# Performance work log

Hardware: AMD Instinct MI355X
Metric: run time of the kernel (lower is better)

## Reference

```python
import jax, jax.numpy as jnp
import numpy as np

B, T, DIM = 4, 1024, 2048
H, KVH = 16, 4
HD = DIM // H          # 128
G = H // KVH           # GQA group size = 4


def setup_inputs() -> dict:
    key = jax.random.key(0)
    ks = jax.random.split(key, 4)
    s = 1.0 / np.sqrt(DIM)
    x = jax.random.normal(ks[0], (B, T, DIM), jnp.float32)
    Wq = jax.random.normal(ks[1], (DIM, DIM), jnp.float32) * s
    Wkv = jax.random.normal(ks[2], (DIM, 2 * KVH * HD), jnp.float32) * s
    Wo = jax.random.normal(ks[3], (DIM, DIM), jnp.float32) * s
    # RoPE tables (theta=10000, half-split / rotate-half convention)
    inv_freq = 1.0 / (10000.0 ** (np.arange(0, HD, 2, dtype=np.float64) / HD))
    freqs = np.outer(np.arange(T, dtype=np.float64), inv_freq)  # [T, HD/2]
    cos = jnp.asarray(np.cos(freqs), jnp.float32)
    sin = jnp.asarray(np.sin(freqs), jnp.float32)
    return {"x": x, "Wq": Wq, "Wkv": Wkv, "Wo": Wo, "cos": cos, "sin": sin}


def _rope(u, cos, sin):
    # u: [B,T,heads,HD]; cos/sin: [T, HD/2]
    u1, u2 = jnp.split(u, 2, axis=-1)
    c = cos[None, :, None, :]
    s = sin[None, :, None, :]
    return jnp.concatenate([u1 * c - u2 * s, u1 * s + u2 * c], axis=-1)


def reference(x, Wq, Wkv, Wo, cos, sin):
    Bs, Ts, C = x.shape
    q = (x @ Wq).reshape(Bs, Ts, H, HD)
    kv = (x @ Wkv).reshape(Bs, Ts, 2, KVH, HD)
    k, v = kv[:, :, 0], kv[:, :, 1]
    q = _rope(q, cos, sin)
    k = _rope(k, cos, sin)
    # GQA without materializing repeated K/V: fold group dim into q
    qg = q.reshape(Bs, Ts, KVH, G, HD)
    scores = jnp.einsum('bqhgd,bkhd->bhgqk', qg, k) / np.float32(np.sqrt(HD))
    causal = jnp.tril(jnp.ones((Ts, Ts), bool))
    neg = jnp.finfo(scores.dtype).min
    scores = jnp.where(causal, scores, neg)
    att = jax.nn.softmax(scores, axis=-1)
    out = jnp.einsum('bhgqk,bkhd->bqhgd', att, v).reshape(Bs, Ts, C)
    return out @ Wo
```

## Files before the change

### kernel.cpp

```cpp
#include <hip/hip_runtime.h>

typedef unsigned short u16;
typedef unsigned int u32;
typedef __bf16 bf16x8 __attribute__((ext_vector_type(8)));
typedef float f32x4 __attribute__((ext_vector_type(4)));

#define BB   4
#define TT   1024
#define CDIM 2048
#define NH   16
#define NKV  4
#define HDIM 128

__device__ __forceinline__ float b2f(u16 u) {
    union { u32 i; float f; } x; x.i = ((u32)u) << 16; return x.f;
}
__device__ __forceinline__ u16 f2b(float f) {
    union { float f; u32 i; } x; x.f = f;
    u32 r = (x.i + 0x7fffu + ((x.i >> 16) & 1u)) >> 16;
    return (u16)r;
}
__device__ __forceinline__ void async16(const void* g, void* l) {
    __builtin_amdgcn_global_load_lds((const __attribute__((address_space(1))) void*)g,
                                     (__attribute__((address_space(3))) void*)l, 16, 0, 0);
}

__device__ __forceinline__ bool wave_is_f32(const u16* xp) {
    u16 v = xp[(threadIdx.x & 63) * 2];
    int e = (v >> 7) & 0xFF;
    bool bad = (v != 0) && (e < 90 || e > 160);
    return __popcll(__ballot(bad)) > 16;
}

__global__ __launch_bounds__(256) void pre_k(const void* __restrict__ x,
                                             const void* __restrict__ Wq,
                                             const void* __restrict__ Wkv,
                                             const void* __restrict__ Wo,
                                             u16* __restrict__ xb,
                                             u16* __restrict__ csb,
                                             u16* __restrict__ snb,
                                             u16* __restrict__ WqkvT,
                                             u16* __restrict__ WoT,
                                             const void* __restrict__ cs,
                                             const void* __restrict__ sn) {
    const bool f32m = wave_is_f32((const u16*)x);
    int bid = blockIdx.x;
    if (bid < 8320) {
        const void* src; u16* dst; int i;
        if (bid < 8192)      { src = x;  dst = xb;  i = bid * 256 + threadIdx.x; }
        else if (bid < 8256) { src = cs; dst = csb; i = (bid - 8192) * 256 + threadIdx.x; }
        else                 { src = sn; dst = snb; i = (bid - 8256) * 256 + threadIdx.x; }
        union { u16 u[4]; ushort4 v; } o;
        if (f32m) {
            float4 f = ((const float4*)src)[i];
            o.u[0] = f2b(f.x); o.u[1] = f2b(f.y); o.u[2] = f2b(f.z); o.u[3] = f2b(f.w);
        } else {
            o.v = ((const ushort4*)src)[i];
        }
        ((ushort4*)dst)[i] = o.v;
        return;
    }
    __shared__ alignas(16) u16 tile[64 * 65];
    int t = bid - 8320;
    const void* W; u16* WT; int rows, cols, bx, by;
    if (t < 1024)      { W = Wq;  WT = WqkvT;                    rows = 2048; cols = 2048; bx = t & 31;  by = t >> 5; }
    else if (t < 1536) { int l = t - 1024; W = Wkv; WT = WqkvT + (long)2048 * 2048; rows = 2048; cols = 1024; bx = l & 15; by = l >> 4; }
    else               { int l = t - 1536; W = Wo;  WT = WoT;  rows = 2048; cols = 2048; bx = l & 31;   by = l >> 5; }
    const int r0 = by * 64, c0 = bx * 64;
#pragma unroll
    for (int i = 0; i < 16; i++) {
        int c = threadIdx.x + i * 256;
        int rr = c >> 6, cc = c & 63;
        long idx = (long)(r0 + rr) * cols + c0 + cc;
        tile[rr * 65 + cc] = f32m ? f2b(((const float*)W)[idx]) : ((const u16*)W)[idx];
    }
    __syncthreads();
#pragma unroll
    for (int i = 0; i < 16; i++) {
        int c = threadIdx.x + i * 256;
        int rr = c >> 6, cc = c & 63;
        WT[(long)(c0 + rr) * rows + r0 + cc] = tile[cc * 65 + rr];
    }
}

__global__ __launch_bounds__(256) void gemm_bt(const u16* __restrict__ A,
                                               const u16* __restrict__ Bt,
                                               void* __restrict__ C,
                                               int M, int N, int Kd,
                                               const u16* __restrict__ xprobe) {
    __shared__ alignas(16) u16 As[128 * 32];
    __shared__ alignas(16) u16 Bs[128 * 32];
    const bool f32m = (xprobe != nullptr) && wave_is_f32(xprobe);
    const int tid = threadIdx.x;
    const int w = tid >> 6, lane = tid & 63;
    const int wm = w >> 1, wn = w & 1;
    const int l16 = lane & 15, quad = lane >> 4;
    const int bm = blockIdx.y, bn = blockIdx.x;
    const long arow0 = (long)bm * 128;
    const long brow0 = (long)bn * 128;
    const int srow = lane >> 2;
    const int schunk = lane & 3;

    f32x4 acc[4][4];
#pragma unroll
    for (int i = 0; i < 4; i++)
#pragma unroll
        for (int j = 0; j < 4; j++) acc[i][j] = {0.f, 0.f, 0.f, 0.f};

    for (int k0 = 0; k0 < Kd; k0 += 32) {
        __syncthreads();
#pragma unroll
        for (int j = 0; j < 2; j++) {
            int r0 = w * 32 + j * 16;
            const u16* gA = A + (arow0 + r0 + srow) * Kd + k0 + schunk * 8;
            async16(gA, &As[r0 * 32]);
            const u16* gB = Bt + (brow0 + r0 + srow) * Kd + k0 + schunk * 8;
            async16(gB, &Bs[r0 * 32]);
        }
        __syncthreads();
        bf16x8 af[4], bfr[4];
#pragma unroll
        for (int mt = 0; mt < 4; mt++)
            af[mt] = *(const bf16x8*)&As[(wm * 64 + mt * 16 + l16) * 32 + quad * 8];
#pragma unroll
        for (int nt = 0; nt < 4; nt++)
            bfr[nt] = *(const bf16x8*)&Bs[(wn * 64 + nt * 16 + l16) * 32 + quad * 8];
#pragma unroll
        for (int mt = 0; mt < 4; mt++)
#pragma unroll
            for (int nt = 0; nt < 4; nt++)
                acc[mt][nt] = __builtin_amdgcn_mfma_f32_16x16x32_bf16(
                    af[mt], bfr[nt], acc[mt][nt], 0, 0, 0);
    }
#pragma unroll
    for (int mt = 0; mt < 4; mt++) {
#pragma unroll
        for (int nt = 0; nt < 4; nt++) {
            int col = bn * 128 + wn * 64 + nt * 16 + l16;
#pragma unroll
            for (int r = 0; r < 4; r++) {
                long row = bm * 128 + wm * 64 + mt * 16 + quad * 4 + r;
                if (f32m) ((float*)C)[row * N + col] = acc[mt][nt][r];
                else      ((u16*)C)[row * N + col] = f2b(acc[mt][nt][r]);
            }
        }
    }
}

__global__ __launch_bounds__(256) void prep_k(const u16* __restrict__ QKVraw,
                                              const u16* __restrict__ cs,
                                              const u16* __restrict__ sn,
                                              u16* __restrict__ Qr,
                                              u16* __restrict__ Kr,
                                              u16* __restrict__ Vt) {
    int bid = blockIdx.x;
    if (bid < 16384) {
        int idx = bid * 256 + threadIdx.x;
        int d = idx & 63;
        int t = (idx >> 6) & (TT - 1);
        int bh = idx >> 16;
        long src = ((long)((bh >> 4) * TT + t)) * 3072 + (bh & 15) * HDIM;
        float u1 = b2f(QKVraw[src + d]), u2 = b2f(QKVraw[src + d + 64]);
        float c = b2f(cs[t * 64 + d]), s = b2f(sn[t * 64 + d]);
        long dst = ((long)bh * TT + t) * HDIM;
        Qr[dst + d] = f2b(u1 * c - u2 * s);
        Qr[dst + d + 64] = f2b(u1 * s + u2 * c);
    } else if (bid < 20480) {
        int idx = (bid - 16384) * 256 + threadIdx.x;
        int d = idx & 63;
        int t = (idx >> 6) & (TT - 1);
        int bk = idx >> 16;
        long src = ((long)((bk >> 2) * TT + t)) * 3072 + 2048 + (bk & 3) * HDIM;
        float u1 = b2f(QKVraw[src + d]), u2 = b2f(QKVraw[src + d + 64]);
        float c = b2f(cs[t * 64 + d]), s = b2f(sn[t * 64 + d]);
        long dst = ((long)bk * TT + t) * HDIM;
        Kr[dst + d] = f2b(u1 * c - u2 * s);
        Kr[dst + d + 64] = f2b(u1 * s + u2 * c);
    } else {
        int idx = (bid - 20480) * 256 + threadIdx.x;
        int t = idx & (TT - 1);
        int d = (idx >> 10) & (HDIM - 1);
        int bk = idx >> 17;
        Vt[idx] = QKVraw[((long)(bk >> 2) * TT + t) * 3072 + 2560 + (bk & 3) * HDIM + d];
    }
}

__global__ __launch_bounds__(256) void attn_kernel(const u16* __restrict__ Q,
                                                   const u16* __restrict__ Kr,
                                                   const u16* __restrict__ Vt,
                                                   u16* __restrict__ O) {
    __shared__ alignas(16) u16 Ks[2][64 * 128];
    __shared__ alignas(16) u16 Vts[2][128 * 64];
    __shared__ alignas(16) u16 Ps[64 * 88];

    const int tid = threadIdx.x, w = tid >> 6, lane = tid & 63;
    const int l16 = lane & 15, quad = lane >> 4;
    const float scale2 = 0.08838834764831845f * 1.4426950408889634f;

#pragma unroll 1
    for (int it = 0; it < 2; it++) {
        const int j = it ? (1023 - (int)blockIdx.x) : (int)blockIdx.x;
        const int qt = 15 - (j >> 6);
        const int bh = j & 63;
        const int b = bh >> 4, h = bh & 15;
        const int kvh = h >> 2;
        const long qrow0 = (long)bh * TT + qt * 64;
        const long krow0 = (long)(b * NKV + kvh) * TT;
        const long vbase = ((long)(b * NKV + kvh) * HDIM) * TT;

        __syncthreads();

#pragma unroll
        for (int i = 0; i < 4; i++) {
            int slot0 = (w * 4 + i) * 64;
            int slot = slot0 + lane;
            int row = slot >> 4, cp = slot & 15;
            int cg = (cp & 8) | ((cp ^ row) & 7);
            async16(Q + (qrow0 + row) * HDIM + cg * 8, &Ks[0][slot0 * 8]);
        }
        asm volatile("s_waitcnt vmcnt(0)" ::: "memory");
        bf16x8 qf[4];
        {
            const int Rq = w * 16 + l16;
#pragma unroll
            for (int ds = 0; ds < 4; ds++) {
                int c = ds * 4 + quad;
                qf[ds] = *(const bf16x8*)&Ks[0][Rq * 128 + ((c & 8) | ((c ^ Rq) & 7)) * 8];
            }
        }
        asm volatile("s_waitcnt lgkmcnt(0)" ::: "memory");

#pragma unroll
        for (int i = 0; i < 4; i++) {
            int slot0 = (w * 4 + i) * 64;
            int slot = slot0 + lane;
            int row = slot >> 4, cp = slot & 15;
            int cg = (cp & 8) | ((cp ^ row) & 7);
            async16(Kr + (krow0 + row) * HDIM + cg * 8, &Ks[0][slot0 * 8]);
        }
#pragma unroll
        for (int i = 0; i < 4; i++) {
            int slot0 = (w * 4 + i) * 64;
            int slot = slot0 + lane;
            int row = slot >> 3, cp = slot & 7;
            int cg = cp ^ (row & 7);
            async16(Vt + vbase + (long)row * TT + cg * 8, &Vts[0][slot0 * 8]);
        }
        if (qt >= 1) {
#pragma unroll
            for (int i = 0; i < 4; i++) {
                int slot0 = (w * 4 + i) * 64;
                int slot = slot0 + lane;
                int row = slot >> 4, cp = slot & 15;
                int cg = (cp & 8) | ((cp ^ row) & 7);
                async16(Kr + (krow0 + 64 + row) * HDIM + cg * 8, &Ks[1][slot0 * 8]);
            }
#pragma unroll
            for (int i = 0; i < 4; i++) {
                int slot0 = (w * 4 + i) * 64;
                int slot = slot0 + lane;
                int row = slot >> 3, cp = slot & 7;
                int cg = cp ^ (row & 7);
                async16(Vt + vbase + (long)row * TT + 64 + cg * 8, &Vts[1][slot0 * 8]);
            }
            asm volatile("s_waitcnt vmcnt(8)" ::: "memory");
        } else {
            asm volatile("s_waitcnt vmcnt(0)" ::: "memory");
        }
        asm volatile("s_barrier" ::: "memory");

        f32x4 o[8];
#pragma unroll
        for (int i = 0; i < 8; i++) o[i] = {0.f, 0.f, 0.f, 0.f};
        float m_i = -1.0e30f, l_i = 0.f;
        const int qg = qt * 64 + w * 16 + l16;

#pragma unroll 1
        for (int kt = 0; kt <= qt; kt++) {
            const int cur = kt & 1;
            const u16* ksb = Ks[cur];
            const u16* vsb = Vts[cur];

            f32x4 s[4];
#pragma unroll
            for (int nt = 0; nt < 4; nt++) s[nt] = {0.f, 0.f, 0.f, 0.f};
#pragma unroll
            for (int ds = 0; ds < 4; ds++) {
                int c = ds * 4 + quad;
#pragma unroll
                for (int nt = 0; nt < 4; nt++) {
                    int Rk = nt * 16 + l16;
                    bf16x8 ak = *(const bf16x8*)&ksb[Rk * 128 + ((c & 8) | ((c ^ Rk) & 7)) * 8];
                    s[nt] = __builtin_amdgcn_mfma_f32_16x16x32_bf16(ak, qf[ds], s[nt], 0, 0, 0);
                }
            }

            float p[4][4];
            float mx = -1.0e30f;
            if (kt == qt) {
#pragma unroll
                for (int nt = 0; nt < 4; nt++)
#pragma unroll
                    for (int r = 0; r < 4; r++) {
                        int kcol = kt * 64 + nt * 16 + quad * 4 + r;
                        float v = (kcol <= qg) ? (float)s[nt][r] * scale2 : -1.0e30f;
                        p[nt][r] = v;
                        mx = fmaxf(mx, v);
                    }
            } else {
#pragma unroll
                for (int nt = 0; nt < 4; nt++)
#pragma unroll
                    for (int r = 0; r < 4; r++) {
                        float v = (float)s[nt][r] * scale2;
                        p[nt][r] = v;
                        mx = fmaxf(mx, v);
                    }
            }
            mx = fmaxf(mx, __shfl_xor(mx, 16));
            mx = fmaxf(mx, __shfl_xor(mx, 32));
            float mnew = fmaxf(m_i, mx);
            float alpha = exp2f(m_i - mnew);
            float rs = 0.f;
#pragma unroll
            for (int nt = 0; nt < 4; nt++)
#pragma unroll
                for (int r = 0; r < 4; r++) {
                    float e = exp2f(p[nt][r] - mnew);
                    p[nt][r] = e;
                    rs += e;
                }
            rs += __shfl_xor(rs, 16);
            rs += __shfl_xor(rs, 32);
            l_i = l_i * alpha + rs;

            u32* Psw = (u32*)Ps;
            int pb = (w * 16 + l16) * 44 + quad * 2;
#pragma unroll
            for (int nt = 0; nt < 4; nt++) {
                u32 lo = (u32)f2b(p[nt][0]) | ((u32)f2b(p[nt][1]) << 16);
                u32 hi = (u32)f2b(p[nt][2]) | ((u32)f2b(p[nt][3]) << 16);
                Psw[pb + nt * 8]     = lo;
                Psw[pb + nt * 8 + 1] = hi;
            }
            if (__ballot(mnew != m_i) != 0ULL) {
#pragma unroll
                for (int n8 = 0; n8 < 8; n8++)
#pragma unroll
                    for (int r = 0; r < 4; r++) o[n8][r] *= alpha;
            }
            m_i = mnew;

            asm volatile("s_waitcnt lgkmcnt(0)" ::: "memory");

#pragma unroll
            for (int ks = 0; ks < 2; ks++) {
                bf16x8 bp = *(const bf16x8*)&Ps[(w * 16 + l16) * 88 + ks * 32 + quad * 8];
#pragma unroll
                for (int n8 = 0; n8 < 8; n8++) {
                    int Rv = n8 * 16 + l16;
                    int c = ks * 4 + quad;
                    bf16x8 av = *(const bf16x8*)&vsb[Rv * 64 + (c ^ (Rv & 7)) * 8];
                    o[n8] = __builtin_amdgcn_mfma_f32_16x16x32_bf16(av, bp, o[n8], 0, 0, 0);
                }
            }

            if (kt == qt) break;

            asm volatile("s_waitcnt lgkmcnt(0)" ::: "memory");
            asm volatile("s_barrier" ::: "memory");
            if (kt + 2 <= qt) {
                const int nk = kt + 2;
#pragma unroll
                for (int i = 0; i < 4; i++) {
                    int slot0 = (w * 4 + i) * 64;
                    int slot = slot0 + lane;
                    int row = slot >> 4, cp = slot & 15;
                    int cg = (cp & 8) | ((cp ^ row) & 7);
                    async16(Kr + (krow0 + nk * 64 + row) * HDIM + cg * 8, &Ks[cur][slot0 * 8]);
                }
#pragma unroll
                for (int i = 0; i < 4; i++) {
                    int slot0 = (w * 4 + i) * 64;
                    int slot = slot0 + lane;
                    int row = slot >> 3, cp = slot & 7;
                    int cg = cp ^ (row & 7);
                    async16(Vt + vbase + (long)row * TT + nk * 64 + cg * 8, &Vts[cur][slot0 * 8]);
                }
                asm volatile("s_waitcnt vmcnt(8)" ::: "memory");
            } else {
                asm volatile("s_waitcnt vmcnt(0)" ::: "memory");
            }
            asm volatile("s_barrier" ::: "memory");
        }

        float inv = 1.0f / l_i;
        long obase = ((long)(b * TT + qg)) * CDIM + h * HDIM;
#pragma unroll
        for (int n8 = 0; n8 < 8; n8++) {
            ushort4 st;
            st.x = f2b(o[n8][0] * inv);
            st.y = f2b(o[n8][1] * inv);
            st.z = f2b(o[n8][2] * inv);
            st.w = f2b(o[n8][3] * inv);
            *(ushort4*)&O[obase + n8 * 16 + quad * 4] = st;
        }
    }
}

extern "C" void kernel_launch(void* const* d_in, const int* in_sizes, int n_in,
                              void* d_out, int out_size, void* d_ws, size_t ws_size,
                              hipStream_t stream) {
    const void* x   = d_in[0];
    const void* Wq  = d_in[1];
    const void* Wkv = d_in[2];
    const void* Wo  = d_in[3];
    const void* cs  = d_in[4];
    const void* sn  = d_in[5];

    char* ws = (char*)d_ws;
    const size_t NEED = 105119748;
    if (ws_size < NEED) return;

    u16* WqkvT = (u16*)(ws + 0);
    u16* WoT   = (u16*)(ws + 12582912);
    u16* QKVraw= (u16*)(ws + 20971520);
    u16* Qr    = (u16*)(ws + 46137344);
    u16* Kr    = (u16*)(ws + 62914560);
    u16* Vt    = (u16*)(ws + 67108864);
    u16* ATT   = (u16*)(ws + 71303168);
    u16* xb    = (u16*)(ws + 88080384);
    u16* csb   = (u16*)(ws + 104857600);
    u16* snb   = (u16*)(ws + 104988672);

    pre_k<<<10880, 256, 0, stream>>>(x, Wq, Wkv, Wo, xb, csb, snb, WqkvT, WoT, cs, sn);

    gemm_bt<<<dim3(24, 32), 256, 0, stream>>>(xb, WqkvT, QKVraw, 4096, 3072, 2048, nullptr);

    prep_k<<<28672, 256, 0, stream>>>(QKVraw, csb, snb, Qr, Kr, Vt);

    attn_kernel<<<512, 256, 0, stream>>>(Qr, Kr, Vt, ATT);

    gemm_bt<<<dim3(16, 32), 256, 0, stream>>>(ATT, WoT, d_out, 4096, 2048, 2048, (const u16*)x);
}
```

Before: 330.1 us.

## Replace GEMM with 256x256 double-buffered swizzled MFMA kernel with phased prefetch

Swaps the 128x128, K=32 GEMM for a 512-thread kernel computing 256x256 tiles with K=64 steps. Loads are double-buffered through direct global-to-LDS copies with an XOR swizzle. Each K step is split into four MFMA phases that interleave LDS fragment reads with prefetch of the next A and B halves, using explicit waitcnt, barriers and priority hints. The aim is more reuse per loaded byte and overlapping memory traffic with matrix math. The trade-off is far fewer blocks than CUs for these shapes, and heavy LDS and register use.

```diff
diff --git a/kernel.cpp b/kernel.cpp
--- a/kernel.cpp
+++ b/kernel.cpp
@@ -83,63 +83,167 @@
     }
 }
 
-__global__ __launch_bounds__(256) void gemm_bt(const u16* __restrict__ A,
-                                               const u16* __restrict__ Bt,
-                                               void* __restrict__ C,
-                                               int M, int N, int Kd,
-                                               const u16* __restrict__ xprobe) {
-    __shared__ alignas(16) u16 As[128 * 32];
-    __shared__ alignas(16) u16 Bs[128 * 32];
+__global__ __launch_bounds__(512, 2) void gemm256(const u16* __restrict__ A,
+                                                  const u16* __restrict__ Bt,
+                                                  void* __restrict__ C,
+                                                  int M, int N, int Kd,
+                                                  const u16* __restrict__ xprobe) {
+    __shared__ alignas(16) u16 As[2][256 * 64];
+    __shared__ alignas(16) u16 Bs[2][256 * 64];
     const bool f32m = (xprobe != nullptr) && wave_is_f32(xprobe);
     const int tid = threadIdx.x;
     const int w = tid >> 6, lane = tid & 63;
-    const int wm = w >> 1, wn = w & 1;
+    const int wm = w >> 2, wn = w & 3;
     const int l16 = lane & 15, quad = lane >> 4;
-    const int bm = blockIdx.y, bn = blockIdx.x;
-    const long arow0 = (long)bm * 128;
-    const long brow0 = (long)bn * 128;
-    const int srow = lane >> 2;
-    const int schunk = lane & 3;
-
-    f32x4 acc[4][4];
-#pragma unroll
-    for (int i = 0; i < 4; i++)
+    const long arow0 = (long)blockIdx.y * 256;
+    const long brow0 = (long)blockIdx.x * 256;
+    const int NT = Kd >> 6;
+
+    long g0, g1;
+    int c0, c1;
+    {
+        int ch = w * 64 + lane;
+        int r = ch >> 3, cp = ch & 7;
+        g0 = (long)r * Kd + ((cp ^ (r & 7)) << 3);
+        c0 = (w * 64) << 3;
+        ch += 512;
+        r = ch >> 3; cp = ch & 7;
+        g1 = (long)r * Kd + ((cp ^ (r & 7)) << 3);
+        c1 = (512 + w * 64) << 3;
+    }
+    const u16* Ab = A + arow0 * Kd;
+    const u16* Bb = Bt + brow0 * Kd;
+    const long halfK = 128L * Kd;
+
+#define STAGE(ldsbase, gbase) do {      \
+        const u16* _g = (gbase);        \
+        u16* _l = (ldsbase);            \
+        async16(_g + g0, _l + c0);      \
+        async16(_g + g1, _l + c1); } while (0)
+
+    const int R0a = wm * 128 + l16, sA = R0a & 7;
+    const int R0b = wn * 64 + l16, sB = R0b & 7;
+    const int aoff[2] = { R0a * 64 + ((quad ^ sA) << 3), R0a * 64 + (((4 + quad) ^ sA) << 3) };
+    const int boff[2] = { R0b * 64 + ((quad ^ sB) << 3), R0b * 64 + (((4 + quad) ^ sB) << 3) };
+
+    f32x4 acc[8][4];
+#pragma unroll
+    for (int i = 0; i < 8; i++)
 #pragma unroll
         for (int j = 0; j < 4; j++) acc[i][j] = {0.f, 0.f, 0.f, 0.f};
 
-    for (int k0 = 0; k0 < Kd; k0 += 32) {
-        __syncthreads();
-#pragma unroll
-        for (int j = 0; j < 2; j++) {
-            int r0 = w * 32 + j * 16;
-            const u16* gA = A + (arow0 + r0 + srow) * Kd + k0 + schunk * 8;
-            async16(gA, &As[r0 * 32]);
-            const u16* gB = Bt + (brow0 + r0 + srow) * Kd + k0 + schunk * 8;
-            async16(gB, &Bs[r0 * 32]);
-        }
-        __syncthreads();
-        bf16x8 af[4], bfr[4];
-#pragma unroll
-        for (int mt = 0; mt < 4; mt++)
-            af[mt] = *(const bf16x8*)&As[(wm * 64 + mt * 16 + l16) * 32 + quad * 8];
-#pragma unroll
-        for (int nt = 0; nt < 4; nt++)
-            bfr[nt] = *(const bf16x8*)&Bs[(wn * 64 + nt * 16 + l16) * 32 + quad * 8];
-#pragma unroll
-        for (int mt = 0; mt < 4; mt++)
-#pragma unroll
-            for (int nt = 0; nt < 4; nt++)
-                acc[mt][nt] = __builtin_amdgcn_mfma_f32_16x16x32_bf16(
-                    af[mt], bfr[nt], acc[mt][nt], 0, 0, 0);
-    }
-#pragma unroll
-    for (int mt = 0; mt < 4; mt++) {
+    STAGE(&Bs[0][0], Bb);
+    STAGE(&Bs[0][128 * 64], Bb + halfK);
+    STAGE(&As[0][0], Ab);
+    STAGE(&As[0][128 * 64], Ab + halfK);
+    STAGE(&Bs[1][0], Bb + 64);
+    STAGE(&Bs[1][128 * 64], Bb + halfK + 64);
+    asm volatile("s_waitcnt vmcnt(4)" ::: "memory");
+    __builtin_amdgcn_s_barrier();
+
+#pragma unroll 1
+    for (int t = 0; t < NT; ++t) {
+        const int cur = t & 1, nxt = cur ^ 1;
+        const u16* pA = &As[cur][0];
+        const u16* pB = &Bs[cur][0];
+        bf16x8 afLo[4][2], afHi[4][2], bfA[2][2], bfB[2][2];
+
+#pragma unroll
+        for (int ks = 0; ks < 2; ks++) {
+#pragma unroll
+            for (int mt = 0; mt < 4; mt++)
+                afLo[mt][ks] = *(const bf16x8*)&pA[aoff[ks] + mt * 1024];
+#pragma unroll
+            for (int nt = 0; nt < 2; nt++)
+                bfA[nt][ks] = *(const bf16x8*)&pB[boff[ks] + nt * 1024];
+        }
+        if (t + 1 < NT) STAGE(&As[nxt][0], Ab + (t + 1) * 64);
+        __builtin_amdgcn_s_barrier();
+        asm volatile("s_waitcnt lgkmcnt(0)" ::: "memory");
+        __builtin_amdgcn_sched_barrier(0);
+        __builtin_amdgcn_s_setprio(1);
+#pragma unroll
+        for (int ks = 0; ks < 2; ks++)
+#pragma unroll
+            for (int mt = 0; mt < 4; mt++)
+#pragma unroll
+                for (int nt = 0; nt < 2; nt++)
+                    acc[mt][nt] = __builtin_amdgcn_mfma_f32_16x16x32_bf16(
+                        afLo[mt][ks], bfA[nt][ks], acc[mt][nt], 0, 0, 0);
+        __builtin_amdgcn_s_setprio(0);
+        __builtin_amdgcn_s_barrier();
+
+#pragma unroll
+        for (int ks = 0; ks < 2; ks++)
+#pragma unroll
+            for (int nt = 0; nt < 2; nt++)
+                bfB[nt][ks] = *(const bf16x8*)&pB[boff[ks] + (nt + 2) * 1024];
+        if (t + 1 < NT) STAGE(&As[nxt][128 * 64], Ab + halfK + (t + 1) * 64);
+        __builtin_amdgcn_s_barrier();
+        asm volatile("s_waitcnt lgkmcnt(0)" ::: "memory");
+        __builtin_amdgcn_sched_barrier(0);
+        __builtin_amdgcn_s_setprio(1);
+#pragma unroll
+        for (int ks = 0; ks < 2; ks++)
+#pragma unroll
+            for (int mt = 0; mt < 4; mt++)
+#pragma unroll
+                for (int nt = 0; nt < 2; nt++)
+                    acc[mt][nt + 2] = __builtin_amdgcn_mfma_f32_16x16x32_bf16(
+                        afLo[mt][ks], bfB[nt][ks], acc[mt][nt + 2], 0, 0, 0);
+        __builtin_amdgcn_s_setprio(0);
+        __builtin_amdgcn_s_barrier();
+
+#pragma unroll
+        for (int ks = 0; ks < 2; ks++)
+#pragma unroll
+            for (int mt = 0; mt < 4; mt++)
+                afHi[mt][ks] = *(const bf16x8*)&pA[aoff[ks] + (mt + 4) * 1024];
+        if (t + 2 < NT) STAGE(&Bs[cur][0], Bb + (t + 2) * 64);
+        __builtin_amdgcn_s_barrier();
+        asm volatile("s_waitcnt lgkmcnt(0)" ::: "memory");
+        __builtin_amdgcn_sched_barrier(0);
+        __builtin_amdgcn_s_setprio(1);
+#pragma unroll
+        for (int ks = 0; ks < 2; ks++)
+#pragma unroll
+            for (int mt = 0; mt < 4; mt++)
+#pragma unroll
+                for (int nt = 0; nt < 2; nt++)
+                    acc[mt + 4][nt + 2] = __builtin_amdgcn_mfma_f32_16x16x32_bf16(
+                        afHi[mt][ks], bfB[nt][ks], acc[mt + 4][nt + 2], 0, 0, 0);
+        __builtin_amdgcn_s_setprio(0);
+        __builtin_amdgcn_s_barrier();
+
+        if (t + 2 < NT) STAGE(&Bs[cur][128 * 64], Bb + halfK + (t + 2) * 64);
+        __builtin_amdgcn_s_barrier();
+        __builtin_amdgcn_sched_barrier(0);
+        __builtin_amdgcn_s_setprio(1);
+#pragma unroll
+        for (int ks = 0; ks < 2; ks++)
+#pragma unroll
+            for (int mt = 0; mt < 4; mt++)
+#pragma unroll
+                for (int nt = 0; nt < 2; nt++)
+                    acc[mt + 4][nt] = __builtin_amdgcn_mfma_f32_16x16x32_bf16(
+                        afHi[mt][ks], bfA[nt][ks], acc[mt + 4][nt], 0, 0, 0);
+        __builtin_amdgcn_s_setprio(0);
+        if (t + 1 < NT) {
+            if (t + 2 < NT) asm volatile("s_waitcnt vmcnt(4)" ::: "memory");
+            else            asm volatile("s_waitcnt vmcnt(0)" ::: "memory");
+            __builtin_amdgcn_s_barrier();
+        }
+    }
+#undef STAGE
+
+#pragma unroll
+    for (int mt = 0; mt < 8; mt++) {
 #pragma unroll
         for (int nt = 0; nt < 4; nt++) {
-            int col = bn * 128 + wn * 64 + nt * 16 + l16;
+            long col = brow0 + wn * 64 + nt * 16 + l16;
 #pragma unroll
             for (int r = 0; r < 4; r++) {
-                long row = bm * 128 + wm * 64 + mt * 16 + quad * 4 + r;
+                long row = arow0 + wm * 128 + mt * 16 + quad * 4 + r;
                 if (f32m) ((float*)C)[row * N + col] = acc[mt][nt][r];
                 else      ((u16*)C)[row * N + col] = f2b(acc[mt][nt][r]);
             }
@@ -435,11 +539,11 @@
 
     pre_k<<<10880, 256, 0, stream>>>(x, Wq, Wkv, Wo, xb, csb, snb, WqkvT, WoT, cs, sn);
 
-    gemm_bt<<<dim3(24, 32), 256, 0, stream>>>(xb, WqkvT, QKVraw, 4096, 3072, 2048, nullptr);
+    gemm256<<<dim3(12, 16), 512, 0, stream>>>(xb, WqkvT, QKVraw, 4096, 3072, 2048, nullptr);
 
     prep_k<<<28672, 256, 0, stream>>>(QKVraw, csb, snb, Qr, Kr, Vt);
 
     attn_kernel<<<512, 256, 0, stream>>>(Qr, Kr, Vt, ATT);
 
-    gemm_bt<<<dim3(16, 32), 256, 0, stream>>>(ATT, WoT, d_out, 4096, 2048, 2048, (const u16*)x);
-}
+    gemm256<<<dim3(8, 16), 512, 0, stream>>>(ATT, WoT, d_out, 4096, 2048, 2048, (const u16*)x);
+}
```

Measured after the change: 323.9 us. About the same (-1.9%).

## Rewrite GEMMs with double-buffered swizzled LDS, larger tiles and split MFMA phases

Applied to the files above, without the earlier changes.

Replaces the single-buffered 128x128, K=32 GEMM with a templated 512-thread kernel that uses K=64 tiles, double-buffered LDS with XOR swizzle, and manual vmcnt/barrier control. Global loads for the next-but-one tile are issued while MFMAs run in two halves, with s_setprio used to favour the math waves. The QKV projection uses 256x192 tiles and the output projection 128x256 tiles. This targets the GEMM loop's load latency and LDS bank conflicts, at the cost of more registers and LDS and fewer blocks (256 per GEMM), which may underfill the CUs.

```diff
diff --git a/kernel.cpp b/kernel.cpp
--- a/kernel.cpp
+++ b/kernel.cpp
@@ -23,6 +23,14 @@
 __device__ __forceinline__ void async16(const void* g, void* l) {
     __builtin_amdgcn_global_load_lds((const __attribute__((address_space(1))) void*)g,
                                      (__attribute__((address_space(3))) void*)l, 16, 0, 0);
+}
+template<int N> __device__ __forceinline__ void waitvm() {
+    static_assert(N == 0 || N == 3 || N == 4 || N == 6 || N == 7, "unsupported vmcnt");
+    if constexpr (N == 0)      asm volatile("s_waitcnt vmcnt(0)" ::: "memory");
+    else if constexpr (N == 3) asm volatile("s_waitcnt vmcnt(3)" ::: "memory");
+    else if constexpr (N == 4) asm volatile("s_waitcnt vmcnt(4)" ::: "memory");
+    else if constexpr (N == 6) asm volatile("s_waitcnt vmcnt(6)" ::: "memory");
+    else                       asm volatile("s_waitcnt vmcnt(7)" ::: "memory");
 }
 
 __device__ __forceinline__ bool wave_is_f32(const u16* xp) {
@@ -83,63 +91,145 @@
     }
 }
 
-__global__ __launch_bounds__(256) void gemm_bt(const u16* __restrict__ A,
-                                               const u16* __restrict__ Bt,
-                                               void* __restrict__ C,
-                                               int M, int N, int Kd,
-                                               const u16* __restrict__ xprobe) {
-    __shared__ alignas(16) u16 As[128 * 32];
-    __shared__ alignas(16) u16 Bs[128 * 32];
+template<int BM, int BN>
+__global__ __launch_bounds__(512, 2) void gemm_t(const u16* __restrict__ A,
+                                                 const u16* __restrict__ Bt,
+                                                 void* __restrict__ C,
+                                                 int N, int Kd,
+                                                 const u16* __restrict__ xprobe) {
+    constexpr int MF  = BM / 32;
+    constexpr int NF  = BN / 64;
+    constexpr int MF0 = MF / 2, MF1 = MF - MF0;
+    constexpr int NF0 = (NF + 1) / 2, NF1 = NF - NF0;
+    constexpr int NAU = BM / 64;
+    constexpr int NBU = BN / 64;
+
+    __shared__ alignas(16) u16 As[2][BM * 64];
+    __shared__ alignas(16) u16 Bs[2][BN * 64];
+
     const bool f32m = (xprobe != nullptr) && wave_is_f32(xprobe);
     const int tid = threadIdx.x;
     const int w = tid >> 6, lane = tid & 63;
-    const int wm = w >> 1, wn = w & 1;
+    const int wm = w >> 2, wn = w & 3;
     const int l16 = lane & 15, quad = lane >> 4;
-    const int bm = blockIdx.y, bn = blockIdx.x;
-    const long arow0 = (long)bm * 128;
-    const long brow0 = (long)bn * 128;
-    const int srow = lane >> 2;
-    const int schunk = lane & 3;
-
-    f32x4 acc[4][4];
-#pragma unroll
-    for (int i = 0; i < 4; i++)
-#pragma unroll
-        for (int j = 0; j < 4; j++) acc[i][j] = {0.f, 0.f, 0.f, 0.f};
-
-    for (int k0 = 0; k0 < Kd; k0 += 32) {
-        __syncthreads();
-#pragma unroll
-        for (int j = 0; j < 2; j++) {
-            int r0 = w * 32 + j * 16;
-            const u16* gA = A + (arow0 + r0 + srow) * Kd + k0 + schunk * 8;
-            async16(gA, &As[r0 * 32]);
-            const u16* gB = Bt + (brow0 + r0 + srow) * Kd + k0 + schunk * 8;
-            async16(gB, &Bs[r0 * 32]);
-        }
-        __syncthreads();
-        bf16x8 af[4], bfr[4];
-#pragma unroll
-        for (int mt = 0; mt < 4; mt++)
-            af[mt] = *(const bf16x8*)&As[(wm * 64 + mt * 16 + l16) * 32 + quad * 8];
-#pragma unroll
-        for (int nt = 0; nt < 4; nt++)
-            bfr[nt] = *(const bf16x8*)&Bs[(wn * 64 + nt * 16 + l16) * 32 + quad * 8];
-#pragma unroll
-        for (int mt = 0; mt < 4; mt++)
-#pragma unroll
-            for (int nt = 0; nt < 4; nt++)
-                acc[mt][nt] = __builtin_amdgcn_mfma_f32_16x16x32_bf16(
-                    af[mt], bfr[nt], acc[mt][nt], 0, 0, 0);
-    }
-#pragma unroll
-    for (int mt = 0; mt < 4; mt++) {
-#pragma unroll
-        for (int nt = 0; nt < 4; nt++) {
-            int col = bn * 128 + wn * 64 + nt * 16 + l16;
+    const long arow0 = (long)blockIdx.y * BM;
+    const long brow0 = (long)blockIdx.x * BN;
+    const int NT = Kd >> 6;
+
+    const int srow = tid >> 3, scp = tid & 7;
+    const long gst = (long)srow * Kd + ((scp ^ (srow & 7)) << 3);
+    const int cst = tid << 3;
+
+    const u16* Ab = A + arow0 * Kd;
+    const u16* Bb = Bt + brow0 * Kd;
+
+    auto stageA = [&](int buf, int t) {
+#pragma unroll
+        for (int u = 0; u < NAU; u++)
+            async16(Ab + (long)u * 64 * Kd + t * 64 + gst, &As[buf][u * 4096 + cst]);
+    };
+    auto stageB = [&](int buf, int t) {
+#pragma unroll
+        for (int u = 0; u < NBU; u++)
+            async16(Bb + (long)u * 64 * Kd + t * 64 + gst, &Bs[buf][u * 4096 + cst]);
+    };
+
+    const int R0a = wm * (BM / 2) + l16, sA = R0a & 7;
+    const int R0b = wn * (BN / 4) + l16, sB = R0b & 7;
+    int aoff[2], boff[2];
+    aoff[0] = R0a * 64 + ((quad ^ sA) << 3);
+    aoff[1] = R0a * 64 + (((4 + quad) ^ sA) << 3);
+    boff[0] = R0b * 64 + ((quad ^ sB) << 3);
+    boff[1] = R0b * 64 + (((4 + quad) ^ sB) << 3);
+
+    f32x4 acc[MF][NF];
+#pragma unroll
+    for (int i = 0; i < MF; i++)
+#pragma unroll
+        for (int j = 0; j < NF; j++) acc[i][j] = {0.f, 0.f, 0.f, 0.f};
+
+    stageB(0, 0); stageA(0, 0); stageB(1, 1); stageA(1, 1);
+    waitvm<NAU + NBU>();
+    __builtin_amdgcn_s_barrier();
+
+#pragma unroll 1
+    for (int t = 0; t < NT; ++t) {
+        const int cur = t & 1;
+        const u16* pA = &As[cur][0];
+        const u16* pB = &Bs[cur][0];
+        bf16x8 afLo[MF0][2], afHi[MF1][2], bfA[NF0][2], bfB[NF1][2];
+
+#pragma unroll
+        for (int ks = 0; ks < 2; ks++) {
+#pragma unroll
+            for (int mt = 0; mt < MF0; mt++)
+                afLo[mt][ks] = *(const bf16x8*)&pA[aoff[ks] + mt * 1024];
+#pragma unroll
+            for (int nt = 0; nt < NF0; nt++)
+                bfA[nt][ks] = *(const bf16x8*)&pB[boff[ks] + nt * 1024];
+#pragma unroll
+            for (int nt = 0; nt < NF1; nt++)
+                bfB[nt][ks] = *(const bf16x8*)&pB[boff[ks] + (NF0 + nt) * 1024];
+        }
+        asm volatile("s_waitcnt lgkmcnt(0)" ::: "memory");
+        __builtin_amdgcn_sched_barrier(0);
+        __builtin_amdgcn_s_setprio(1);
+#pragma unroll
+        for (int ks = 0; ks < 2; ks++)
+#pragma unroll
+            for (int mt = 0; mt < MF0; mt++) {
+#pragma unroll
+                for (int nt = 0; nt < NF0; nt++)
+                    acc[mt][nt] = __builtin_amdgcn_mfma_f32_16x16x32_bf16(
+                        afLo[mt][ks], bfA[nt][ks], acc[mt][nt], 0, 0, 0);
+#pragma unroll
+                for (int nt = 0; nt < NF1; nt++)
+                    acc[mt][NF0 + nt] = __builtin_amdgcn_mfma_f32_16x16x32_bf16(
+                        afLo[mt][ks], bfB[nt][ks], acc[mt][NF0 + nt], 0, 0, 0);
+            }
+        __builtin_amdgcn_s_setprio(0);
+
+#pragma unroll
+        for (int ks = 0; ks < 2; ks++)
+#pragma unroll
+            for (int mt = 0; mt < MF1; mt++)
+                afHi[mt][ks] = *(const bf16x8*)&pA[aoff[ks] + (MF0 + mt) * 1024];
+        __builtin_amdgcn_s_barrier();
+        if (t + 2 < NT) stageB(cur, t + 2);
+        asm volatile("s_waitcnt lgkmcnt(0)" ::: "memory");
+        __builtin_amdgcn_sched_barrier(0);
+        __builtin_amdgcn_s_setprio(1);
+#pragma unroll
+        for (int ks = 0; ks < 2; ks++)
+#pragma unroll
+            for (int mt = 0; mt < MF1; mt++) {
+#pragma unroll
+                for (int nt = 0; nt < NF1; nt++)
+                    acc[MF0 + mt][NF0 + nt] = __builtin_amdgcn_mfma_f32_16x16x32_bf16(
+                        afHi[mt][ks], bfB[nt][ks], acc[MF0 + mt][NF0 + nt], 0, 0, 0);
+#pragma unroll
+                for (int nt = 0; nt < NF0; nt++)
+                    acc[MF0 + mt][nt] = __builtin_amdgcn_mfma_f32_16x16x32_bf16(
+                        afHi[mt][ks], bfA[nt][ks], acc[MF0 + mt][nt], 0, 0, 0);
+            }
+        __builtin_amdgcn_s_setprio(0);
+
+        if (t + 1 < NT) {
+            if (t + 2 < NT) waitvm<NBU>();
+            else            waitvm<0>();
+            __builtin_amdgcn_s_barrier();
+            if (t + 2 < NT) stageA(cur, t + 2);
+        }
+    }
+
+#pragma unroll
+    for (int mt = 0; mt < MF; mt++) {
+#pragma unroll
+        for (int nt = 0; nt < NF; nt++) {
+            long col = brow0 + wn * (BN / 4) + nt * 16 + l16;
 #pragma unroll
             for (int r = 0; r < 4; r++) {
-                long row = bm * 128 + wm * 64 + mt * 16 + quad * 4 + r;
+                long row = arow0 + wm * (BM / 2) + mt * 16 + quad * 4 + r;
                 if (f32m) ((float*)C)[row * N + col] = acc[mt][nt][r];
                 else      ((u16*)C)[row * N + col] = f2b(acc[mt][nt][r]);
             }
@@ -435,11 +525,11 @@
 
     pre_k<<<10880, 256, 0, stream>>>(x, Wq, Wkv, Wo, xb, csb, snb, WqkvT, WoT, cs, sn);
 
-    gemm_bt<<<dim3(24, 32), 256, 0, stream>>>(xb, WqkvT, QKVraw, 4096, 3072, 2048, nullptr);
+    gemm_t<256, 192><<<dim3(16, 16), 512, 0, stream>>>(xb, WqkvT, QKVraw, 3072, 2048, nullptr);
 
     prep_k<<<28672, 256, 0, stream>>>(QKVraw, csb, snb, Qr, Kr, Vt);
 
     attn_kernel<<<512, 256, 0, stream>>>(Qr, Kr, Vt, ATT);
 
-    gemm_bt<<<dim3(16, 32), 256, 0, stream>>>(ATT, WoT, d_out, 4096, 2048, 2048, (const u16*)x);
-}
+    gemm_t<128, 256><<<dim3(8, 32), 512, 0, stream>>>(ATT, WoT, d_out, 2048, 2048, (const u16*)x);
+}
```

Result: faster. 302.5 us (-8.4%).

## Replace 128x128 GEMM with 256x256 double-buffered pipelined MFMA kernel

Applied to the files above, without the earlier changes.

Replaces the simple 128x128-tile bf16 GEMM with a 512-thread, 256x256-tile kernel that uses K=64 steps, double-buffered LDS with XOR-swizzled layout, and async global-to-LDS staging interleaved with the MFMA phases. Manual waitcnt/barrier placement and s_setprio are meant to overlap memory loads with compute and reduce LDS bank conflicts and per-k synchronisation overhead. The larger tiles raise per-block reuse but launch far fewer blocks (192 and 128) on a 256-CU device, which risks underfilling the GPU. The hand-written waitcnt sequencing is also fragile.

```diff
diff --git a/kernel.cpp b/kernel.cpp
--- a/kernel.cpp
+++ b/kernel.cpp
@@ -83,63 +83,177 @@
     }
 }
 
-__global__ __launch_bounds__(256) void gemm_bt(const u16* __restrict__ A,
-                                               const u16* __restrict__ Bt,
-                                               void* __restrict__ C,
-                                               int M, int N, int Kd,
-                                               const u16* __restrict__ xprobe) {
-    __shared__ alignas(16) u16 As[128 * 32];
-    __shared__ alignas(16) u16 Bs[128 * 32];
+__global__ __launch_bounds__(512, 2) void gemm256(const u16* __restrict__ A,
+                                                  const u16* __restrict__ Bt,
+                                                  void* __restrict__ C,
+                                                  int N, int Kd,
+                                                  const u16* __restrict__ xprobe) {
+    __shared__ alignas(16) u16 As[2][2][128 * 64];
+    __shared__ alignas(16) u16 Bs[2][2][128 * 64];
     const bool f32m = (xprobe != nullptr) && wave_is_f32(xprobe);
     const int tid = threadIdx.x;
     const int w = tid >> 6, lane = tid & 63;
-    const int wm = w >> 1, wn = w & 1;
+    const int wm = w >> 2, wn = w & 3;
     const int l16 = lane & 15, quad = lane >> 4;
-    const int bm = blockIdx.y, bn = blockIdx.x;
-    const long arow0 = (long)bm * 128;
-    const long brow0 = (long)bn * 128;
-    const int srow = lane >> 2;
-    const int schunk = lane & 3;
-
-    f32x4 acc[4][4];
-#pragma unroll
-    for (int i = 0; i < 4; i++)
+    const long arow0 = (long)blockIdx.y * 256;
+    const long brow0 = (long)blockIdx.x * 256;
+    const int NT = Kd >> 6;
+
+    long gs0, gs1; int lo0, lo1;
+    {
+        int ch = tid, r = ch >> 3, cp = ch & 7;
+        gs0 = (long)r * Kd + ((cp ^ (r & 7)) << 3);
+        lo0 = ch << 3;
+        ch = tid + 512; r = ch >> 3; cp = ch & 7;
+        gs1 = (long)r * Kd + ((cp ^ (r & 7)) << 3);
+        lo1 = ch << 3;
+    }
+    const u16* Ab = A + arow0 * Kd;
+    const u16* Bb = Bt + brow0 * Kd;
+    const long halfK = 128L * Kd;
+
+#define STAGEH(ldsbase, gbase) do {        \
+        const u16* _g = (gbase);           \
+        u16* _l = (ldsbase);               \
+        async16(_g + gs0, _l + lo0);       \
+        async16(_g + gs1, _l + lo1); } while (0)
+#define BARRIER() asm volatile("s_barrier" ::: "memory")
+#define LGKM0()   asm volatile("s_waitcnt lgkmcnt(0)" ::: "memory")
+#define LGKM8()   asm volatile("s_waitcnt lgkmcnt(8)" ::: "memory")
+
+    const int sw = l16 & 7;
+    int aoff[2], boff[2];
+    aoff[0] = l16 * 64 + ((quad ^ sw) << 3);
+    aoff[1] = l16 * 64 + (((4 + quad) ^ sw) << 3);
+    boff[0] = ((wn & 1) * 64 + l16) * 64 + ((quad ^ sw) << 3);
+    boff[1] = ((wn & 1) * 64 + l16) * 64 + (((4 + quad) ^ sw) << 3);
+    const int bh = wn >> 1;
+
+    f32x4 acc[8][4];
+#pragma unroll
+    for (int i = 0; i < 8; i++)
 #pragma unroll
         for (int j = 0; j < 4; j++) acc[i][j] = {0.f, 0.f, 0.f, 0.f};
 
-    for (int k0 = 0; k0 < Kd; k0 += 32) {
-        __syncthreads();
-#pragma unroll
-        for (int j = 0; j < 2; j++) {
-            int r0 = w * 32 + j * 16;
-            const u16* gA = A + (arow0 + r0 + srow) * Kd + k0 + schunk * 8;
-            async16(gA, &As[r0 * 32]);
-            const u16* gB = Bt + (brow0 + r0 + srow) * Kd + k0 + schunk * 8;
-            async16(gB, &Bs[r0 * 32]);
-        }
-        __syncthreads();
-        bf16x8 af[4], bfr[4];
-#pragma unroll
-        for (int mt = 0; mt < 4; mt++)
-            af[mt] = *(const bf16x8*)&As[(wm * 64 + mt * 16 + l16) * 32 + quad * 8];
-#pragma unroll
-        for (int nt = 0; nt < 4; nt++)
-            bfr[nt] = *(const bf16x8*)&Bs[(wn * 64 + nt * 16 + l16) * 32 + quad * 8];
-#pragma unroll
-        for (int mt = 0; mt < 4; mt++)
-#pragma unroll
-            for (int nt = 0; nt < 4; nt++)
-                acc[mt][nt] = __builtin_amdgcn_mfma_f32_16x16x32_bf16(
-                    af[mt], bfr[nt], acc[mt][nt], 0, 0, 0);
-    }
-#pragma unroll
-    for (int mt = 0; mt < 4; mt++) {
+    bf16x8 afLo[4][2], afHi[4][2], bfA[2][2], bfB[2][2];
+
+    STAGEH(&Bs[0][0][0], Bb);
+    STAGEH(&Bs[0][1][0], Bb + halfK);
+    STAGEH(&As[0][0][0], Ab);
+    STAGEH(&As[0][1][0], Ab + halfK);
+    STAGEH(&Bs[1][0][0], Bb + 64);
+    STAGEH(&As[1][0][0], Ab + 64);
+    asm volatile("s_waitcnt vmcnt(4)" ::: "memory");
+    BARRIER();
+
+#define KTILE(T, CUR, NXT)                                                      \
+    {                                                                           \
+        const u16* pA = &As[CUR][wm][0];                                        \
+        const u16* pB = &Bs[CUR][bh][0];                                        \
+                     \
+        _Pragma("unroll")                                                       \
+        for (int ks = 0; ks < 2; ks++) {                                        \
+            _Pragma("unroll")                                                   \
+            for (int mt = 0; mt < 4; mt++)                                      \
+                afLo[mt][ks] = *(const bf16x8*)&pA[aoff[ks] + mt * 1024];       \
+            _Pragma("unroll")                                                   \
+            for (int nt = 0; nt < 2; nt++)                                      \
+                bfA[nt][ks] = *(const bf16x8*)&pB[boff[ks] + nt * 1024];        \
+        }                                                                       \
+        if ((T) + 1 < NT) STAGEH(&Bs[NXT][1][0], Bb + halfK + ((T) + 1) * 64);  \
+        LGKM8();                                                                \
+        BARRIER();                                                              \
+        LGKM0();                                                                \
+        __builtin_amdgcn_s_setprio(1);                                          \
+        _Pragma("unroll")                                                       \
+        for (int ks = 0; ks < 2; ks++)                                          \
+            _Pragma("unroll")                                                   \
+            for (int mt = 0; mt < 4; mt++)                                      \
+                _Pragma("unroll")                                               \
+                for (int nt = 0; nt < 2; nt++)                                  \
+                    acc[mt][nt] = __builtin_amdgcn_mfma_f32_16x16x32_bf16(      \
+                        afLo[mt][ks], bfA[nt][ks], acc[mt][nt], 0, 0, 0);       \
+        __builtin_amdgcn_s_setprio(0);                                          \
+        BARRIER();                                                              \
+                           \
+        _Pragma("unroll")                                                       \
+        for (int ks = 0; ks < 2; ks++)                                          \
+            _Pragma("unroll")                                                   \
+            for (int nt = 0; nt < 2; nt++)                                      \
+                bfB[nt][ks] = *(const bf16x8*)&pB[boff[ks] + (nt + 2) * 1024];  \
+        if ((T) + 1 < NT) STAGEH(&As[NXT][1][0], Ab + halfK + ((T) + 1) * 64);  \
+        BARRIER();                                                              \
+        LGKM0();                                                                \
+        __builtin_amdgcn_s_setprio(1);                                          \
+        _Pragma("unroll")                                                       \
+        for (int ks = 0; ks < 2; ks++)                                          \
+            _Pragma("unroll")                                                   \
+            for (int mt = 0; mt < 4; mt++)                                      \
+                _Pragma("unroll")                                               \
+                for (int nt = 0; nt < 2; nt++)                                  \
+                    acc[mt][nt + 2] = __builtin_amdgcn_mfma_f32_16x16x32_bf16(  \
+                        afLo[mt][ks], bfB[nt][ks], acc[mt][nt + 2], 0, 0, 0);   \
+        __builtin_amdgcn_s_setprio(0);                                          \
+        BARRIER();                                                              \
+                          \
+        _Pragma("unroll")                                                       \
+        for (int ks = 0; ks < 2; ks++)                                          \
+            _Pragma("unroll")                                                   \
+            for (int mt = 0; mt < 4; mt++)                                      \
+                afHi[mt][ks] = *(const bf16x8*)&pA[aoff[ks] + (mt + 4) * 1024]; \
+        if ((T) + 2 < NT) STAGEH(&Bs[CUR][0][0], Bb + ((T) + 2) * 64);          \
+        BARRIER();                                                              \
+        LGKM0();                                                                \
+        __builtin_amdgcn_s_setprio(1);                                          \
+        _Pragma("unroll")                                                       \
+        for (int ks = 0; ks < 2; ks++)                                          \
+            _Pragma("unroll")                                                   \
+            for (int mt = 0; mt < 4; mt++)                                      \
+                _Pragma("unroll")                                               \
+                for (int nt = 0; nt < 2; nt++)                                  \
+                    acc[mt + 4][nt + 2] = __builtin_amdgcn_mfma_f32_16x16x32_bf16( \
+                        afHi[mt][ks], bfB[nt][ks], acc[mt + 4][nt + 2], 0, 0, 0);  \
+        __builtin_amdgcn_s_setprio(0);                                          \
+        BARRIER();                                                              \
+               \
+        if ((T) + 2 < NT) STAGEH(&As[CUR][0][0], Ab + ((T) + 2) * 64);          \
+        BARRIER();                                                              \
+        __builtin_amdgcn_s_setprio(1);                                          \
+        _Pragma("unroll")                                                       \
+        for (int ks = 0; ks < 2; ks++)                                          \
+            _Pragma("unroll")                                                   \
+            for (int mt = 0; mt < 4; mt++)                                      \
+                _Pragma("unroll")                                               \
+                for (int nt = 0; nt < 2; nt++)                                  \
+                    acc[mt + 4][nt] = __builtin_amdgcn_mfma_f32_16x16x32_bf16(  \
+                        afHi[mt][ks], bfA[nt][ks], acc[mt + 4][nt], 0, 0, 0);   \
+        __builtin_amdgcn_s_setprio(0);                                          \
+        if ((T) + 1 < NT) {                                                     \
+            if ((T) + 2 < NT) asm volatile("s_waitcnt vmcnt(4)" ::: "memory");  \
+            else              asm volatile("s_waitcnt vmcnt(0)" ::: "memory");  \
+        }                                                                       \
+        BARRIER();                                                              \
+    }
+
+#pragma unroll 1
+    for (int t = 0; t < NT; t += 2) {
+        KTILE(t, 0, 1);
+        KTILE(t + 1, 1, 0);
+    }
+#undef KTILE
+#undef STAGEH
+#undef BARRIER
+#undef LGKM0
+#undef LGKM8
+
+#pragma unroll
+    for (int mt = 0; mt < 8; mt++) {
 #pragma unroll
         for (int nt = 0; nt < 4; nt++) {
-            int col = bn * 128 + wn * 64 + nt * 16 + l16;
+            long col = brow0 + wn * 64 + nt * 16 + l16;
 #pragma unroll
             for (int r = 0; r < 4; r++) {
-                long row = bm * 128 + wm * 64 + mt * 16 + quad * 4 + r;
+                long row = arow0 + wm * 128 + mt * 16 + quad * 4 + r;
                 if (f32m) ((float*)C)[row * N + col] = acc[mt][nt][r];
                 else      ((u16*)C)[row * N + col] = f2b(acc[mt][nt][r]);
             }
@@ -435,11 +549,11 @@
 
     pre_k<<<10880, 256, 0, stream>>>(x, Wq, Wkv, Wo, xb, csb, snb, WqkvT, WoT, cs, sn);
 
-    gemm_bt<<<dim3(24, 32), 256, 0, stream>>>(xb, WqkvT, QKVraw, 4096, 3072, 2048, nullptr);
+    gemm256<<<dim3(12, 16), 512, 0, stream>>>(xb, WqkvT, QKVraw, 3072, 2048, nullptr);
 
     prep_k<<<28672, 256, 0, stream>>>(QKVraw, csb, snb, Qr, Kr, Vt);
 
     attn_kernel<<<512, 256, 0, stream>>>(Qr, Kr, Vt, ATT);
 
-    gemm_bt<<<dim3(16, 32), 256, 0, stream>>>(ATT, WoT, d_out, 4096, 2048, 2048, (const u16*)x);
-}
+    gemm256<<<dim3(8, 16), 512, 0, stream>>>(ATT, WoT, d_out, 2048, 2048, (const u16*)x);
+}
```

Measured after the change: 329.8 us. Within noise of the previous version (-0.1%).
